# Performance work log

Hardware: AMD Instinct MI355X
Metric: run time of the kernel (lower is better)

Reference implementation:

```python
import jax, jax.numpy as jnp
import numpy as np

B, T, F, H, O = 256, 1024, 128, 512, 64
BN_EPS = 1e-5


def setup_inputs() -> dict:
    key = jax.random.key(0)
    ks = jax.random.split(key, 24)
    p = lambda k, shape: 0.02 * jax.random.normal(k, shape, dtype=jnp.float32)
    inp = {
        "x": jax.random.normal(ks[0], (B, T, F), dtype=jnp.float32),
        "delta": jax.random.uniform(ks[1], (B, T, F), dtype=jnp.float32),
        "m": (jax.random.uniform(ks[2], (B, T, F)) > 0.5).astype(jnp.float32),
        "x_forward": jax.random.normal(ks[3], (B, T, F), dtype=jnp.float32),
        # packed-sequence style: descending number of active rows per timestep
        "batch_sizes": jnp.sort(jax.random.randint(ks[4], (T,), 1, B + 1))[::-1].astype(jnp.int32),
        "W_r": p(ks[5], (F, H)), "U_r": p(ks[6], (H, H)), "V_r": p(ks[7], (F, H)), "b_r": jnp.zeros((H,), jnp.float32),
        "W_z": p(ks[8], (F, H)), "U_z": p(ks[9], (H, H)), "V_z": p(ks[10], (F, H)), "b_z": jnp.zeros((H,), jnp.float32),
        "W": p(ks[11], (F, H)), "U": p(ks[12], (H, H)), "V": p(ks[13], (F, H)), "b": jnp.zeros((H,), jnp.float32),
        "W_gamma_x": p(ks[14], (F,)), "b_gamma_x": jnp.zeros((F,), jnp.float32),
        "W_gamma_h": p(ks[15], (F, H)), "b_gamma_h": jnp.zeros((H,), jnp.float32),
        "dec_W": p(ks[16], (H, O)), "dec_b": jnp.zeros((O,), jnp.float32),
        "bn_w": jnp.ones((H,), jnp.float32), "bn_b": jnp.zeros((H,), jnp.float32),
    }
    return inp


def reference(x, delta, m, x_forward, batch_sizes,
              W_r, U_r, V_r, b_r, W_z, U_z, V_z, b_z, W, U, V, b,
              W_gamma_x, b_gamma_x, W_gamma_h, b_gamma_h,
              dec_W, dec_b, bn_w, bn_b):
    # input decay gamma_x: [B,T,F]; hidden decay gamma_h: [B,T,H]
    gamma_x = jnp.exp(-jax.nn.relu(delta * W_gamma_x + b_gamma_x))
    gamma_h = jnp.exp(-jax.nn.relu(jnp.einsum("btf,fh->bth", m, W_gamma_h) + b_gamma_h))
    # impute observed (m==1) positions with decayed forward-fill (matches x[m.byte()] = x_replace[m.byte()])
    x_rep = gamma_x * x_forward + (1.0 - gamma_x) * 0.001
    x = jnp.where(m > 0.5, x_rep, x)

    # time-major for scan
    xT = jnp.transpose(x, (1, 0, 2))        # [T,B,F]
    mT = jnp.transpose(m, (1, 0, 2))        # [T,B,F]
    gT = jnp.transpose(gamma_h, (1, 0, 2))  # [T,B,H]
    row = jnp.arange(B)

    def step(h, inp):
        x_t, m_t, g_t, bs = inp
        mask = (row < bs)[:, None]          # active rows this step
        h_d = jnp.where(mask, g_t * h, h)   # decayed hidden (index_copy_ on [:bs])
        one_m = 1.0 - m_t
        z = jax.nn.sigmoid(x_t @ W_z + h_d @ U_z + one_m @ V_z + b_z)
        r = jax.nn.sigmoid(x_t @ W_r + h_d @ U_r + one_m @ V_r + b_r)
        h_tilde = jnp.tanh(x_t @ W + (h_d * r) @ U + one_m @ V + b)
        h_new = jnp.where(mask, (1.0 - z) * h_d + z * h_tilde, h_d)
        return h_new, None

    h0 = jnp.zeros((B, H), jnp.float32)
    h_t, _ = jax.lax.scan(step, h0, (xT, mT, gT, batch_sizes))

    # eval-mode BatchNorm1d (running_mean=0, running_var=1); batch_size>1 so BN applies
    h_bn = h_t * (bn_w / jnp.sqrt(1.0 + BN_EPS)) + bn_b
    output = jax.nn.log_softmax(h_bn @ dec_W + dec_b, axis=-1)
    return output, h_bn
```

## Files before the change

### kernel.cpp

```cpp
#include <hip/hip_runtime.h>
#include <hip/hip_bf16.h>

typedef __attribute__((ext_vector_type(8))) short bf16x8;
typedef __attribute__((ext_vector_type(4))) float f32x4;
typedef __attribute__((ext_vector_type(4))) float fvec4;
typedef __attribute__((ext_vector_type(4))) unsigned short u16x4;
typedef __attribute__((ext_vector_type(4))) int i32x4;
typedef __attribute__((ext_vector_type(2))) unsigned int u32x2;

#define DEVI __device__ __forceinline__

constexpr int BB = 256, TT = 1024, FF = 128, HH = 512, OO = 64;
constexpr int KK = 256;
constexpr int NN = 2048;

DEVI unsigned short f2bf(float x) {
  unsigned int u = __float_as_uint(x);
  u += 0x7FFFu + ((u >> 16) & 1u);
  return (unsigned short)(u >> 16);
}
DEVI float bf2f(unsigned short s) {
  return __uint_as_float(((unsigned int)s) << 16);
}

DEVI void gload16(const void* g, void* lds) {
  __builtin_amdgcn_global_load_lds(
      (const __attribute__((address_space(1))) void*)g,
      (__attribute__((address_space(3))) void*)lds, 16, 0, 0);
}

DEVI void barrier_lds() {
  asm volatile("s_waitcnt lgkmcnt(0)" ::: "memory");
  __builtin_amdgcn_s_barrier();
  __builtin_amdgcn_sched_barrier(0);
}

DEVI int hgIdx(int row, int c) { return row*1024 + (c ^ ((row & 7) << 3)); }

__global__ __launch_bounds__(256) void prep_scales_kernel(
    const float* __restrict__ U_z, const float* __restrict__ U_r,
    const float* __restrict__ Uh, float* __restrict__ uscale)
{
  int n = blockIdx.x * 256 + threadIdx.x;
  if (n >= 1536) return;
  const float* src = (n < 512) ? U_z : (n < 1024) ? U_r : Uh;
  int col = n & 511;
  float s = 0.f;
  for (int k = 0; k < HH; ++k) s = fmaxf(s, fabsf(src[k*HH + col]));
  uscale[n] = fmaxf(s, 1e-30f);
}

__global__ __launch_bounds__(256) void prep_kernel(
    const float* __restrict__ W_z, const float* __restrict__ V_z, const float* __restrict__ b_z,
    const float* __restrict__ W_r, const float* __restrict__ V_r, const float* __restrict__ b_r,
    const float* __restrict__ Wh,  const float* __restrict__ Vh,  const float* __restrict__ bh,
    const float* __restrict__ Wgh, const float* __restrict__ bgh,
    const float* __restrict__ U_z, const float* __restrict__ U_r, const float* __restrict__ Uh,
    const float* __restrict__ uscale,
    unsigned short* __restrict__ BwT, float* __restrict__ bias,
    unsigned int* __restrict__ UzrN, unsigned int* __restrict__ UhN)
{
  int idx = blockIdx.x * 256 + threadIdx.x;
  if (idx < 524288) {
    int n = idx >> 8, k = idx & 255;
    float v;
    if (n < 512)       { int h = n;        v = (k < 128) ? W_z[k*HH + h] : -V_z[(k-128)*HH + h]; }
    else if (n < 1024) { int h = n - 512;  v = (k < 128) ? W_r[k*HH + h] : -V_r[(k-128)*HH + h]; }
    else if (n < 1536) { int h = n - 1024; v = (k < 128) ? Wh [k*HH + h] : -Vh [(k-128)*HH + h]; }
    else               { int h = n - 1536; v = (k < 128) ? 0.f : Wgh[(k-128)*HH + h]; }
    BwT[n*256 + k] = f2bf(v);
    return;
  }
  idx -= 524288;
  if (idx < 2048) {
    int n = idx; float v;
    if (n < 512)       { float s = b_z[n];      for (int f = 0; f < FF; ++f) s += V_z[f*HH + n];        v = s; }
    else if (n < 1024) { int h = n-512;  float s = b_r[h]; for (int f = 0; f < FF; ++f) s += V_r[f*HH + h]; v = s; }
    else if (n < 1536) { int h = n-1024; float s = bh[h];  for (int f = 0; f < FF; ++f) s += Vh[f*HH + h];  v = s; }
    else               { v = bgh[n-1536]; }
    bias[n] = v;
    return;
  }
  idx -= 2048;
  if (idx < 65536) {
    int c  = idx & 1;
    int l  = (idx >> 1) & 63;
    int i  = (idx >> 7) & 3;
    int wv = (idx >> 9) & 7;
    int u  = idx >> 12;
    int kt = u >> 1, half = u & 1;
    int col = (wv*4 + i)*16 + (l & 15);
    const float* src = half ? U_r : U_z;
    float sc = 7.f / uscale[half*512 + col];
    unsigned int word = 0;
#pragma unroll
    for (int p = 0; p < 8; ++p) {
      int j = c*8 + (p & 1)*4 + (p >> 1);
      int k = kt*64 + (l >> 4)*16 + j;
      float q = fminf(fmaxf(rintf(src[k*HH + col] * sc), -7.f), 7.f);
      unsigned int uq = (unsigned int)((int)q + 8);
      word |= (uq & 0xF) << (4*p);
    }
    UzrN[idx] = word;
    return;
  }
  idx -= 65536;
  if (idx < 32768) {
    int c  = idx & 1;
    int l  = (idx >> 1) & 63;
    int i  = (idx >> 7) & 3;
    int wv = (idx >> 9) & 7;
    int u  = idx >> 12;
    int col = (wv*4 + i)*16 + (l & 15);
    float sc = 7.f / uscale[1024 + col];
    unsigned int word = 0;
#pragma unroll
    for (int p = 0; p < 8; ++p) {
      int j = c*8 + (p & 1)*4 + (p >> 1);
      int k = u*64 + (l >> 4)*16 + j;
      float q = fminf(fmaxf(rintf(Uh[k*HH + col] * sc), -7.f), 7.f);
      unsigned int uq = (unsigned int)((int)q + 8);
      word |= (uq & 0xF) << (4*p);
    }
    UhN[idx] = word;
  }
}

__global__ __launch_bounds__(256) void build_A_kernel(
    const float* __restrict__ x, const float* __restrict__ delta,
    const float* __restrict__ mm, const float* __restrict__ xf,
    const float* __restrict__ Wgx, const float* __restrict__ bgx,
    const int* __restrict__ bs, unsigned short* __restrict__ A,
    int t0, int TC)
{
  int blk = blockIdx.x;
  int row8 = blk * 8;
  int b0  = row8 / TC;
  int tl0 = row8 % TC;
  if (b0 >= bs[t0 + tl0]) return;
  int tid = threadIdx.x;
  int rl = row8 + (tid >> 5);
  int tc = tl0 + (tid >> 5);
  long gi = ((long)b0*TT + t0 + tc) * 32 + (tid & 31);
  int f0 = (tid & 31) * 4;
  fvec4 xv = ((const fvec4*)x)[gi];
  fvec4 dv = ((const fvec4*)delta)[gi];
  fvec4 mv = ((const fvec4*)mm)[gi];
  fvec4 fv = ((const fvec4*)xf)[gi];
  unsigned short ox[4], om[4];
#pragma unroll
  for (int j = 0; j < 4; ++j) {
    float g  = __expf(-fmaxf(dv[j]*Wgx[f0+j] + bgx[f0+j], 0.f));
    float xr = g*fv[j] + (1.f - g)*0.001f;
    float xi = (mv[j] > 0.5f) ? xr : xv[j];
    ox[j] = f2bf(xi); om[j] = f2bf(mv[j]);
  }
  *(u16x4*)(A + (long)rl*KK + f0)       = (u16x4){ox[0], ox[1], ox[2], ox[3]};
  *(u16x4*)(A + (long)rl*KK + 128 + f0) = (u16x4){om[0], om[1], om[2], om[3]};
}

__global__ __launch_bounds__(256) void gemm1_kernel(
    const unsigned short* __restrict__ A, const unsigned short* __restrict__ BwT,
    const float* __restrict__ bias, const int* __restrict__ bs,
    unsigned short* __restrict__ PRE, int t0, int TC)
{
  int blk = blockIdx.x;
  int nt = blk & 15;
  int mt = blk >> 4;
  {
    int m0 = mt * 128;
    int b_ = m0 / TC;
    int bcheck = (TC >= 128) ? bs[t0 + (m0 % TC)] : bs[t0];
    if (b_ >= bcheck) return;
  }
  int tid = threadIdx.x;
  int w = tid >> 6, l = tid & 63;
  int wm = w >> 1, wn = w & 1;
  int lr = l & 15, lg = l >> 4;
  int m_base = mt*128 + wm*64;
  int n_base = nt*128 + wn*64;
  const unsigned short* Aptr = A   + (long)(m_base + lr)*KK + lg*8;
  const unsigned short* Bptr = BwT + (long)(n_base + lr)*KK + lg*8;
  f32x4 acc[4][4];
#pragma unroll
  for (int i = 0; i < 4; ++i)
#pragma unroll
    for (int j = 0; j < 4; ++j) acc[i][j] = (f32x4){0.f, 0.f, 0.f, 0.f};

#pragma unroll
  for (int kt = 0; kt < 8; ++kt) {
    bf16x8 af[4], bfr[4];
#pragma unroll
    for (int i = 0; i < 4; ++i) af[i]  = *(const bf16x8*)(Aptr + (long)i*16*KK + kt*32);
#pragma unroll
    for (int i = 0; i < 4; ++i) bfr[i] = *(const bf16x8*)(Bptr + (long)i*16*KK + kt*32);
#pragma unroll
    for (int ms = 0; ms < 4; ++ms)
#pragma unroll
      for (int ns = 0; ns < 4; ++ns)
        acc[ms][ns] = __builtin_amdgcn_mfma_f32_16x16x32_bf16(af[ms], bfr[ns], acc[ms][ns], 0, 0, 0);
  }
#pragma unroll
  for (int ms = 0; ms < 4; ++ms) {
    int gm0 = m_base + ms*16 + lg*4;
#pragma unroll
    for (int ns = 0; ns < 4; ++ns) {
      int gn = n_base + ns*16 + lr;
      float bv = bias[gn];
      bool is_gamma = (gn >= 1536);
#pragma unroll
      for (int q = 0; q < 4; ++q) {
        float v = acc[ms][ns][q] + bv;
        if (is_gamma) v = __expf(-fmaxf(v, 0.f));
        PRE[(long)(gm0 + q)*NN + gn] = f2bf(v);
      }
    }
  }
}

__global__ __launch_bounds__(512, 2) void scan_kernel(
    const unsigned short* __restrict__ PRE,
    const unsigned int* __restrict__ UzrN,
    const unsigned int* __restrict__ UhN,
    const float* __restrict__ uscale,
    const int* __restrict__ bs,
    float* __restrict__ h_st,
    float* __restrict__ sbuf,
    int t0, int TC)
{
  __shared__ __align__(16) char Ubuf[8][4][2048];
  __shared__ __align__(16) i32x4 hd_l[8*64];
  __shared__ __align__(16) unsigned short slabHG[16*1024];
  __shared__ float hm[16][524];
  __shared__ int hsumW[8][16];
  __shared__ int hsumW2[8][16];
  __shared__ float wmax[8];

  const int tid = threadIdx.x;
  const int r0 = blockIdx.x * 16;
  if (t0 > 0 && bs[t0] <= r0) return;

  const int w = tid >> 6, l = tid & 63, lr = l & 15, lg = l >> 4;
  const size_t rowStr = (size_t)TC * NN;

  auto STAGEB = [&](int u) {
    const char* src = (const char*)UhN + ((size_t)(u*8 + w))*2048 + (size_t)l*16;
    char* dst = &Ubuf[w][u & 3][0];
    gload16(src, dst);
    gload16(src + 1024, dst + 1024);
  };
  auto STAGEHG = [&](const unsigned short* PREn) {
#pragma unroll
    for (int j = 0; j < 4; ++j) {
      int idx = w*4 + j;
      int row = idx >> 1;
      int phys = (idx & 1)*512 + l*8;
      int logi = phys ^ ((row & 7) << 3);
      const unsigned short* src = PREn + (size_t)row*rowStr + 1024 + logi;
      gload16(src, &slabHG[idx*512]);
    }
  };
  auto LOADZR = [&](int u, u32x2* d) {
#pragma unroll
    for (int i = 0; i < 4; ++i)
      d[i] = ((const u32x2*)UzrN)[((u*8 + w)*4 + i)*64 + l];
  };

  float zdq[4], rdq[4], hdq[4];
#pragma unroll
  for (int i = 0; i < 4; ++i) {
    int c = (w*4 + i)*16 + lr;
    zdq[i] = uscale[c]        * (1.f/889.f);
    rdq[i] = uscale[512 + c]  * (1.f/889.f);
    hdq[i] = uscale[1024 + c] * (1.f/889.f);
  }
  if (tid < 8) wmax[tid] = (t0 == 0) ? 1e-20f : sbuf[blockIdx.x];

  if (t0 == 0) {
    for (int i = tid; i < 16*512; i += 512) hm[i>>9][i&511] = 0.f;
  } else {
    for (int i = tid; i < 16*512; i += 512)
      hm[i>>9][i&511] = h_st[(size_t)(r0 + (i>>9))*HH + (i&511)];
  }
  asm volatile("s_waitcnt vmcnt(0)" ::: "memory");
  __builtin_amdgcn_sched_barrier(0);

  STAGEHG(PRE + (size_t)r0*TC*NN);
  STAGEB(0); STAGEB(1);

  for (int tc = 0; tc < TC; ++tc) {
    const int bsv = bs[t0 + tc];
    if (bsv <= r0) break;
    const int na = min(16, bsv - r0);
    const unsigned short* PREstep = PRE + ((size_t)r0*TC + tc)*NN;
    const unsigned short* PREnext = PREstep + NN;

    barrier_lds();
    asm volatile("s_waitcnt vmcnt(4)" ::: "memory");
    __builtin_amdgcn_sched_barrier(0);

    float s = wmax[0];
#pragma unroll
    for (int i = 1; i < 8; ++i) s = fmaxf(s, wmax[i]);
    const float qs = 127.f / s;

    unsigned short pzr[2][4][4];
#pragma unroll
    for (int i = 0; i < 4; ++i)
#pragma unroll
      for (int q = 0; q < 4; ++q) {
        int row = lg*4 + q, col = (w*4 + i)*16 + lr;
        const unsigned short* pb = PREstep + (size_t)row*rowStr + col;
        pzr[0][i][q] = pb[0];
        pzr[1][i][q] = pb[512];
      }

    u32x2 inW[4][4];
    LOADZR(0, inW[0]); LOADZR(1, inW[1]);
    LOADZR(2, inW[2]); LOADZR(3, inW[3]);

    i32x4 qwReg;
    {
      const int k0 = w*64 + lg*16;
      const bool act = lr < na;
      bf16x8 g0 = *(const bf16x8*)&slabHG[hgIdx(lr, 512 + k0)];
      bf16x8 g1 = *(const bf16x8*)&slabHG[hgIdx(lr, 512 + k0 + 8)];
      int psum = 0;
#pragma unroll
      for (int d = 0; d < 4; ++d) {
        int word = 0;
#pragma unroll
        for (int b = 0; b < 4; ++b) {
          int j = d*4 + b;
          float h  = hm[lr][k0 + j];
          float gv = bf2f((unsigned short)(j < 8 ? g0[j] : g1[j-8]));
          float hd = act ? gv*h : h;
          float q  = fminf(fmaxf(rintf(hd*qs), -127.f), 127.f);
          int qi = (int)q;
          psum += qi;
          word |= (qi & 0xFF) << (8*b);
        }
        qwReg[d] = word;
      }
      hd_l[w*64 + l] = qwReg;
      psum += __shfl_xor(psum, 16);
      psum += __shfl_xor(psum, 32);
      if (lg == 0) hsumW[w][lr] = psum;
    }

    float phv[4][4], ggv[4][4];
#pragma unroll
    for (int i = 0; i < 4; ++i)
#pragma unroll
      for (int q = 0; q < 4; ++q) {
        int row = lg*4 + q, col = (w*4 + i)*16 + lr;
        phv[i][q] = bf2f(slabHG[hgIdx(row, col)]);
        ggv[i][q] = bf2f(slabHG[hgIdx(row, 512 + col)]);
      }
    barrier_lds();

    i32x4 acc[8];
#pragma unroll
    for (int i = 0; i < 8; ++i) acc[i] = (i32x4){0, 0, 0, 0};
    i32x4 af;
#pragma unroll
    for (int u = 0; u < 16; ++u) {
      if (!(u & 1)) af = hd_l[(u>>1)*64 + l];
      u32x2* inw = inW[u & 3];
      __builtin_amdgcn_s_setprio(1);
#pragma unroll
      for (int i = 0; i < 4; ++i) {
        unsigned int W0 = inw[i][0], W1 = inw[i][1];
        i32x4 bfr;
        bfr[0] = (int)(W0 & 0x0F0F0F0Fu);
        bfr[1] = (int)((W0 >> 4) & 0x0F0F0F0Fu);
        bfr[2] = (int)(W1 & 0x0F0F0F0Fu);
        bfr[3] = (int)((W1 >> 4) & 0x0F0F0F0Fu);
        acc[(u&1)*4 + i] = __builtin_amdgcn_mfma_i32_16x16x64_i8(af, bfr, acc[(u&1)*4 + i], 0, 0, 0);
      }
      __builtin_amdgcn_s_setprio(0);
      if (u < 12) LOADZR(u + 4, inW[u & 3]);
    }
    STAGEB(2); STAGEB(3);

    int rsum[4];
#pragma unroll
    for (int q = 0; q < 4; ++q) {
      int row = lg*4 + q, t = 0;
#pragma unroll
      for (int w2 = 0; w2 < 8; ++w2) t += hsumW[w2][row];
      rsum[q] = t * 8;
    }
    float zreg[4][4];
#pragma unroll
    for (int i = 0; i < 4; ++i)
#pragma unroll
      for (int q = 0; q < 4; ++q) {
        int row = lg*4 + q, col = (w*4 + i)*16 + lr;
        float az = bf2f(pzr[0][i][q]) + (float)(acc[i][q]   - rsum[q]) * zdq[i] * s;
        float ar = bf2f(pzr[1][i][q]) + (float)(acc[4+i][q] - rsum[q]) * rdq[i] * s;
        zreg[i][q] = 1.f/(1.f + __expf(-az));
        slabHG[hgIdx(row, col)] = f2bf(1.f/(1.f + __expf(-ar)));
      }
    barrier_lds();

    {
      const int k0 = w*64 + lg*16;
      bf16x8 r0v = *(const bf16x8*)&slabHG[hgIdx(lr, k0)];
      bf16x8 r1v = *(const bf16x8*)&slabHG[hgIdx(lr, k0 + 8)];
      i32x4 nw;
      int psum2 = 0;
#pragma unroll
      for (int d = 0; d < 4; ++d) {
        int word = qwReg[d], out = 0;
#pragma unroll
        for (int b = 0; b < 4; ++b) {
          int j = d*4 + b;
          int hq = (int)(signed char)((word >> (8*b)) & 0xFF);
          float rv = bf2f((unsigned short)(j < 8 ? r0v[j] : r1v[j-8]));
          float q = fminf(fmaxf(rintf((float)hq * rv), -127.f), 127.f);
          int qi = (int)q;
          psum2 += qi;
          out |= (qi & 0xFF) << (8*b);
        }
        nw[d] = out;
      }
      hd_l[w*64 + l] = nw;
      psum2 += __shfl_xor(psum2, 16);
      psum2 += __shfl_xor(psum2, 32);
      if (lg == 0) hsumW2[w][lr] = psum2;
    }
    barrier_lds();

    i32x4 accB[4];
#pragma unroll
    for (int i = 0; i < 4; ++i) accB[i] = (i32x4){0, 0, 0, 0};
#pragma unroll
    for (int u = 0; u < 8; ++u) {
      if (u < 5) { asm volatile("s_waitcnt vmcnt(6)" ::: "memory"); }
      else       { asm volatile("s_waitcnt vmcnt(8)" ::: "memory"); }
      __builtin_amdgcn_sched_barrier(0);
      const char* buf = &Ubuf[w][u & 3][0];
      i32x4 af2 = hd_l[u*64 + l];
      __builtin_amdgcn_s_setprio(1);
#pragma unroll
      for (int i = 0; i < 4; ++i) {
        u32x2 Wv = *(const u32x2*)&buf[(i*64 + l)*8];
        unsigned int W0 = Wv[0], W1 = Wv[1];
        i32x4 bfr;
        bfr[0] = (int)(W0 & 0x0F0F0F0Fu);
        bfr[1] = (int)((W0 >> 4) & 0x0F0F0F0Fu);
        bfr[2] = (int)(W1 & 0x0F0F0F0Fu);
        bfr[3] = (int)((W1 >> 4) & 0x0F0F0F0Fu);
        accB[i] = __builtin_amdgcn_mfma_i32_16x16x64_i8(af2, bfr, accB[i], 0, 0, 0);
      }
      __builtin_amdgcn_s_setprio(0);
      __builtin_amdgcn_sched_barrier(0);
      if (u < 4)       STAGEB(u + 4);
      else if (u == 4) STAGEHG(PREnext);
      else if (u == 5) STAGEB(0);
      else if (u == 6) STAGEB(1);
    }

    int rsum2[4];
#pragma unroll
    for (int q = 0; q < 4; ++q) {
      int row = lg*4 + q, t = 0;
#pragma unroll
      for (int w2 = 0; w2 < 8; ++w2) t += hsumW2[w2][row];
      rsum2[q] = t * 8;
    }
    float mloc = 0.f;
#pragma unroll
    for (int i = 0; i < 4; ++i)
#pragma unroll
      for (int q = 0; q < 4; ++q) {
        int row = lg*4 + q, col = (w*4 + i)*16 + lr;
        float hval;
        if (row < na) {
          float ah = phv[i][q] + (float)(accB[i][q] - rsum2[q]) * hdq[i] * s;
          float e  = __expf(2.f*ah);
          float th = 1.f - 2.f/(e + 1.f);
          float hd = ggv[i][q] * hm[row][col];
          hval = hd + zreg[i][q]*(th - hd);
          hm[row][col] = hval;
        } else {
          hval = hm[row][col];
        }
        mloc = fmaxf(mloc, fabsf(hval));
      }
#pragma unroll
    for (int off = 32; off > 0; off >>= 1) mloc = fmaxf(mloc, __shfl_xor(mloc, off));
    if (l == 0) wmax[w] = fmaxf(mloc, 1e-20f);
  }

  asm volatile("s_waitcnt vmcnt(0)" ::: "memory");
  barrier_lds();
  for (int i = tid; i < 16*512; i += 512)
    h_st[(size_t)(r0 + (i>>9))*HH + (i&511)] = hm[i>>9][i&511];
  if (tid == 0) {
    float s = wmax[0];
#pragma unroll
    for (int i = 1; i < 8; ++i) s = fmaxf(s, wmax[i]);
    sbuf[blockIdx.x] = s;
  }
}

__global__ __launch_bounds__(64) void head_kernel(
    const float* __restrict__ h_state, const float* __restrict__ decW,
    const float* __restrict__ decb, const float* __restrict__ bnw,
    const float* __restrict__ bnb, float* __restrict__ out)
{
  int b = blockIdx.x, o = threadIdx.x;
  __shared__ float hbn[HH];
  const float s = rsqrtf(1.f + 1e-5f);
  for (int j = o; j < HH; j += 64)
    hbn[j] = h_state[(long)b*HH + j] * (bnw[j] * s) + bnb[j];
  __syncthreads();
  float acc = decb[o];
  for (int j = 0; j < HH; ++j) acc += hbn[j] * decW[j*OO + o];
  float mx = acc;
#pragma unroll
  for (int off = 32; off > 0; off >>= 1) mx = fmaxf(mx, __shfl_xor(mx, off));
  float ex = __expf(acc - mx);
  float sum = ex;
#pragma unroll
  for (int off = 32; off > 0; off >>= 1) sum += __shfl_xor(sum, off);
  out[(long)b*OO + o] = acc - mx - __logf(sum);
  for (int j = o; j < HH; j += 64)
    out[(long)BB*OO + (long)b*HH + j] = hbn[j];
}

extern "C" void kernel_launch(void* const* d_in, const int* in_sizes, int n_in,
                              void* d_out, int out_size, void* d_ws, size_t ws_size,
                              hipStream_t stream) {
  const float* x     = (const float*)d_in[0];
  const float* delta = (const float*)d_in[1];
  const float* mm    = (const float*)d_in[2];
  const float* xf    = (const float*)d_in[3];
  const int*   bs    = (const int*)  d_in[4];
  const float* W_r   = (const float*)d_in[5];
  const float* U_r   = (const float*)d_in[6];
  const float* V_r   = (const float*)d_in[7];
  const float* b_r   = (const float*)d_in[8];
  const float* W_z   = (const float*)d_in[9];
  const float* U_z   = (const float*)d_in[10];
  const float* V_z   = (const float*)d_in[11];
  const float* b_z   = (const float*)d_in[12];
  const float* W     = (const float*)d_in[13];
  const float* U     = (const float*)d_in[14];
  const float* V     = (const float*)d_in[15];
  const float* b     = (const float*)d_in[16];
  const float* Wgx   = (const float*)d_in[17];
  const float* bgx   = (const float*)d_in[18];
  const float* Wgh   = (const float*)d_in[19];
  const float* bgh   = (const float*)d_in[20];
  const float* decW  = (const float*)d_in[21];
  const float* decb  = (const float*)d_in[22];
  const float* bnw   = (const float*)d_in[23];
  const float* bnb   = (const float*)d_in[24];

  auto rnd = [](size_t v) { return (v + 255) & ~(size_t)255; };
  const size_t fixed_bytes = rnd((size_t)2048*256*2) + rnd(2048*4)
                           + rnd((size_t)256*1024) + rnd((size_t)128*1024)
                           + rnd(1536*4) + rnd(64)
                           + rnd((size_t)BB*HH*4);
  int TC = 0;
  const int cands[5] = {128, 64, 32, 16, 8};
  for (int i = 0; i < 5; ++i) {
    size_t need = fixed_bytes + rnd((size_t)BB*cands[i]*KK*2) + rnd((size_t)BB*cands[i]*NN*2);
    if (need <= ws_size) { TC = cands[i]; break; }
  }
  if (TC == 0) return;

  char* p = (char*)d_ws;
  auto alloc = [&](size_t bytes) { char* r = p; p += (bytes + 255) & ~(size_t)255; return r; };
  unsigned short* A_chunk = (unsigned short*)alloc((size_t)BB * TC * KK * 2);
  unsigned short* PREc    = (unsigned short*)alloc((size_t)BB * TC * NN * 2);
  unsigned short* BwT     = (unsigned short*)alloc((size_t)2048 * 256 * 2);
  float*          bias    = (float*)alloc(2048 * 4);
  unsigned int*   UzrN    = (unsigned int*)alloc((size_t)256 * 1024);
  unsigned int*   UhN     = (unsigned int*)alloc((size_t)128 * 1024);
  float*          uscale  = (float*)alloc(1536 * 4);
  float*          sbuf    = (float*)alloc(64);
  float*          h_st    = (float*)alloc((size_t)BB * HH * 4);

  prep_scales_kernel<<<6, 256, 0, stream>>>(U_z, U_r, U, uscale);
  prep_kernel<<<2440, 256, 0, stream>>>(W_z, V_z, b_z, W_r, V_r, b_r, W, V, b,
                                        Wgh, bgh, U_z, U_r, U, uscale,
                                        BwT, bias, UzrN, UhN);
  const int nch = TT / TC;
  for (int c = 0; c < nch; ++c) {
    int t0 = c * TC;
    build_A_kernel<<<BB*TC/8, 256, 0, stream>>>(x, delta, mm, xf, Wgx, bgx, bs,
                                                A_chunk, t0, TC);
    gemm1_kernel<<<(BB*TC/128)*16, 256, 0, stream>>>(A_chunk, BwT, bias, bs,
                                                     PREc, t0, TC);
    scan_kernel<<<16, 512, 0, stream>>>(PREc, UzrN, UhN, uscale, bs,
                                        h_st, sbuf, t0, TC);
  }
  head_kernel<<<256, 64, 0, stream>>>(h_st, decW, decb, bnw, bnb, (float*)d_out);
}
```

Measured before the change: 19.58 ms.

## Stream U_h weights directly into registers instead of LDS staging buffers

Removes the per-wave LDS staging buffer for the U_h int4 weights and instead loads them straight from global memory into registers, prefetching two steps ahead and interleaved with the z/r MFMA loop. The z/r weight prefetch is restructured into a copy-then-reload register rotation. The top-of-step wait now drains all memory counters before the barrier, and the clamp to ±127 in requantization is dropped. This cuts LDS footprint and LDS traffic and may raise occupancy, at the cost of more VGPRs and a full vmcnt(0) stall each step. Removing the clamp risks int8 wraparound if values exceed the range.

```diff
diff --git a/kernel.cpp b/kernel.cpp
--- a/kernel.cpp
+++ b/kernel.cpp
@@ -228,7 +228,6 @@
     float* __restrict__ sbuf,
     int t0, int TC)
 {
-  __shared__ __align__(16) char Ubuf[8][4][2048];
   __shared__ __align__(16) i32x4 hd_l[8*64];
   __shared__ __align__(16) unsigned short slabHG[16*1024];
   __shared__ float hm[16][524];
@@ -243,12 +242,6 @@
   const int w = tid >> 6, l = tid & 63, lr = l & 15, lg = l >> 4;
   const size_t rowStr = (size_t)TC * NN;
 
-  auto STAGEB = [&](int u) {
-    const char* src = (const char*)UhN + ((size_t)(u*8 + w))*2048 + (size_t)l*16;
-    char* dst = &Ubuf[w][u & 3][0];
-    gload16(src, dst);
-    gload16(src + 1024, dst + 1024);
-  };
   auto STAGEHG = [&](const unsigned short* PREn) {
 #pragma unroll
     for (int j = 0; j < 4; ++j) {
@@ -263,7 +256,12 @@
   auto LOADZR = [&](int u, u32x2* d) {
 #pragma unroll
     for (int i = 0; i < 4; ++i)
-      d[i] = ((const u32x2*)UzrN)[((u*8 + w)*4 + i)*64 + l];
+      d[i] = ((const u32x2*)UzrN)[(u*8 + w)*256 + i*64 + l];
+  };
+  auto LOADB = [&](int u, u32x2* d) {
+#pragma unroll
+    for (int i = 0; i < 4; ++i)
+      d[i] = ((const u32x2*)UhN)[(u*8 + w)*256 + i*64 + l];
   };
 
   float zdq[4], rdq[4], hdq[4];
@@ -286,7 +284,9 @@
   __builtin_amdgcn_sched_barrier(0);
 
   STAGEHG(PRE + (size_t)r0*TC*NN);
-  STAGEB(0); STAGEB(1);
+
+  u32x2 inZ[4][4];
+  u32x2 inB[2][4];
 
   for (int tc = 0; tc < TC; ++tc) {
     const int bsv = bs[t0 + tc];
@@ -295,8 +295,9 @@
     const unsigned short* PREstep = PRE + ((size_t)r0*TC + tc)*NN;
     const unsigned short* PREnext = PREstep + NN;
 
-    barrier_lds();
-    asm volatile("s_waitcnt vmcnt(4)" ::: "memory");
+    asm volatile("s_waitcnt lgkmcnt(0)" ::: "memory");
+    asm volatile("s_waitcnt vmcnt(0)" ::: "memory");
+    __builtin_amdgcn_s_barrier();
     __builtin_amdgcn_sched_barrier(0);
 
     float s = wmax[0];
@@ -315,9 +316,8 @@
         pzr[1][i][q] = pb[512];
       }
 
-    u32x2 inW[4][4];
-    LOADZR(0, inW[0]); LOADZR(1, inW[1]);
-    LOADZR(2, inW[2]); LOADZR(3, inW[3]);
+    LOADZR(0, inZ[0]); LOADZR(1, inZ[1]);
+    LOADZR(2, inZ[2]); LOADZR(3, inZ[3]);
 
     i32x4 qwReg;
     {
@@ -335,8 +335,7 @@
           float h  = hm[lr][k0 + j];
           float gv = bf2f((unsigned short)(j < 8 ? g0[j] : g1[j-8]));
           float hd = act ? gv*h : h;
-          float q  = fminf(fmaxf(rintf(hd*qs), -127.f), 127.f);
-          int qi = (int)q;
+          int qi = (int)rintf(hd*qs);
           psum += qi;
           word |= (qi & 0xFF) << (8*b);
         }
@@ -366,11 +365,16 @@
 #pragma unroll
     for (int u = 0; u < 16; ++u) {
       if (!(u & 1)) af = hd_l[(u>>1)*64 + l];
-      u32x2* inw = inW[u & 3];
+      u32x2 cur[4];
+#pragma unroll
+      for (int i = 0; i < 4; ++i) cur[i] = inZ[u & 3][i];
+      if (u < 12)       LOADZR(u + 4, inZ[u & 3]);
+      else if (u == 14) LOADB(0, inB[0]);
+      else if (u == 15) LOADB(1, inB[1]);
       __builtin_amdgcn_s_setprio(1);
 #pragma unroll
       for (int i = 0; i < 4; ++i) {
-        unsigned int W0 = inw[i][0], W1 = inw[i][1];
+        unsigned int W0 = cur[i][0], W1 = cur[i][1];
         i32x4 bfr;
         bfr[0] = (int)(W0 & 0x0F0F0F0Fu);
         bfr[1] = (int)((W0 >> 4) & 0x0F0F0F0Fu);
@@ -379,9 +383,7 @@
         acc[(u&1)*4 + i] = __builtin_amdgcn_mfma_i32_16x16x64_i8(af, bfr, acc[(u&1)*4 + i], 0, 0, 0);
       }
       __builtin_amdgcn_s_setprio(0);
-      if (u < 12) LOADZR(u + 4, inW[u & 3]);
-    }
-    STAGEB(2); STAGEB(3);
+    }
 
     int rsum[4];
 #pragma unroll
@@ -418,8 +420,7 @@
           int j = d*4 + b;
           int hq = (int)(signed char)((word >> (8*b)) & 0xFF);
           float rv = bf2f((unsigned short)(j < 8 ? r0v[j] : r1v[j-8]));
-          float q = fminf(fmaxf(rintf((float)hq * rv), -127.f), 127.f);
-          int qi = (int)q;
+          int qi = (int)rintf((float)hq * rv);
           psum2 += qi;
           out |= (qi & 0xFF) << (8*b);
         }
@@ -437,16 +438,16 @@
     for (int i = 0; i < 4; ++i) accB[i] = (i32x4){0, 0, 0, 0};
 #pragma unroll
     for (int u = 0; u < 8; ++u) {
-      if (u < 5) { asm volatile("s_waitcnt vmcnt(6)" ::: "memory"); }
-      else       { asm volatile("s_waitcnt vmcnt(8)" ::: "memory"); }
-      __builtin_amdgcn_sched_barrier(0);
-      const char* buf = &Ubuf[w][u & 3][0];
+      u32x2 cur[4];
+#pragma unroll
+      for (int i = 0; i < 4; ++i) cur[i] = inB[u & 1][i];
+      if (u < 6)       LOADB(u + 2, inB[u & 1]);
+      if (u == 4)      STAGEHG(PREnext);
       i32x4 af2 = hd_l[u*64 + l];
       __builtin_amdgcn_s_setprio(1);
 #pragma unroll
       for (int i = 0; i < 4; ++i) {
-        u32x2 Wv = *(const u32x2*)&buf[(i*64 + l)*8];
-        unsigned int W0 = Wv[0], W1 = Wv[1];
+        unsigned int W0 = cur[i][0], W1 = cur[i][1];
         i32x4 bfr;
         bfr[0] = (int)(W0 & 0x0F0F0F0Fu);
         bfr[1] = (int)((W0 >> 4) & 0x0F0F0F0Fu);
@@ -455,11 +456,6 @@
         accB[i] = __builtin_amdgcn_mfma_i32_16x16x64_i8(af2, bfr, accB[i], 0, 0, 0);
       }
       __builtin_amdgcn_s_setprio(0);
-      __builtin_amdgcn_sched_barrier(0);
-      if (u < 4)       STAGEB(u + 4);
-      else if (u == 4) STAGEHG(PREnext);
-      else if (u == 5) STAGEB(0);
-      else if (u == 6) STAGEB(1);
     }
 
     int rsum2[4];
```

After: 25.10 ms. +28.2%, slower.

## Double scan kernel block to 1024 threads, halving per-wave column tiles

Applied to the files above, without the earlier changes.

The recurrent scan kernel now runs 16 waves per block instead of 8. Each wave owns two 16-column tiles instead of four, and the weight packing layout is reindexed to match. The aim is to cut the serial per-timestep latency by spreading the int8/int4 MFMA work and gate math over more waves. In exchange, the quantisation and h_d packing stages run on only half the waves, barriers span more waves, and the int8 clamp was dropped, which risks overflow if a value rounds past 127.

```diff
diff --git a/kernel.cpp b/kernel.cpp
--- a/kernel.cpp
+++ b/kernel.cpp
@@ -85,11 +85,10 @@
   if (idx < 65536) {
     int c  = idx & 1;
     int l  = (idx >> 1) & 63;
-    int i  = (idx >> 7) & 3;
-    int wv = (idx >> 9) & 7;
+    int t  = (idx >> 7) & 31;
     int u  = idx >> 12;
     int kt = u >> 1, half = u & 1;
-    int col = (wv*4 + i)*16 + (l & 15);
+    int col = t*16 + (l & 15);
     const float* src = half ? U_r : U_z;
     float sc = 7.f / uscale[half*512 + col];
     unsigned int word = 0;
@@ -108,10 +107,9 @@
   if (idx < 32768) {
     int c  = idx & 1;
     int l  = (idx >> 1) & 63;
-    int i  = (idx >> 7) & 3;
-    int wv = (idx >> 9) & 7;
+    int t  = (idx >> 7) & 31;
     int u  = idx >> 12;
-    int col = (wv*4 + i)*16 + (l & 15);
+    int col = t*16 + (l & 15);
     float sc = 7.f / uscale[1024 + col];
     unsigned int word = 0;
 #pragma unroll
@@ -218,7 +216,7 @@
   }
 }
 
-__global__ __launch_bounds__(512, 2) void scan_kernel(
+__global__ __launch_bounds__(1024) void scan_kernel(
     const unsigned short* __restrict__ PRE,
     const unsigned int* __restrict__ UzrN,
     const unsigned int* __restrict__ UhN,
@@ -228,13 +226,13 @@
     float* __restrict__ sbuf,
     int t0, int TC)
 {
-  __shared__ __align__(16) char Ubuf[8][4][2048];
+  __shared__ __align__(16) char Ubuf[16][4][1024];
   __shared__ __align__(16) i32x4 hd_l[8*64];
   __shared__ __align__(16) unsigned short slabHG[16*1024];
   __shared__ float hm[16][524];
   __shared__ int hsumW[8][16];
   __shared__ int hsumW2[8][16];
-  __shared__ float wmax[8];
+  __shared__ float wmax[16];
 
   const int tid = threadIdx.x;
   const int r0 = blockIdx.x * 16;
@@ -244,42 +242,38 @@
   const size_t rowStr = (size_t)TC * NN;
 
   auto STAGEB = [&](int u) {
-    const char* src = (const char*)UhN + ((size_t)(u*8 + w))*2048 + (size_t)l*16;
-    char* dst = &Ubuf[w][u & 3][0];
-    gload16(src, dst);
-    gload16(src + 1024, dst + 1024);
+    const char* src = (const char*)UhN + ((size_t)(u*32 + w*2))*512 + (size_t)l*16;
+    gload16(src, &Ubuf[w][u & 3][0]);
   };
   auto STAGEHG = [&](const unsigned short* PREn) {
 #pragma unroll
-    for (int j = 0; j < 4; ++j) {
-      int idx = w*4 + j;
-      int row = idx >> 1;
-      int phys = (idx & 1)*512 + l*8;
-      int logi = phys ^ ((row & 7) << 3);
-      const unsigned short* src = PREn + (size_t)row*rowStr + 1024 + logi;
-      gload16(src, &slabHG[idx*512]);
+    for (int j = 0; j < 2; ++j) {
+      int phys = j*512 + l*8;
+      int logi = phys ^ ((w & 7) << 3);
+      const unsigned short* src = PREn + (size_t)w*rowStr + 1024 + logi;
+      gload16(src, &slabHG[(w*2 + j)*512]);
     }
   };
   auto LOADZR = [&](int u, u32x2* d) {
 #pragma unroll
-    for (int i = 0; i < 4; ++i)
-      d[i] = ((const u32x2*)UzrN)[((u*8 + w)*4 + i)*64 + l];
+    for (int i = 0; i < 2; ++i)
+      d[i] = ((const u32x2*)UzrN)[(u*32 + w*2 + i)*64 + l];
   };
 
-  float zdq[4], rdq[4], hdq[4];
-#pragma unroll
-  for (int i = 0; i < 4; ++i) {
-    int c = (w*4 + i)*16 + lr;
+  float zdq[2], rdq[2], hdq[2];
+#pragma unroll
+  for (int i = 0; i < 2; ++i) {
+    int c = (w*2 + i)*16 + lr;
     zdq[i] = uscale[c]        * (1.f/889.f);
     rdq[i] = uscale[512 + c]  * (1.f/889.f);
     hdq[i] = uscale[1024 + c] * (1.f/889.f);
   }
-  if (tid < 8) wmax[tid] = (t0 == 0) ? 1e-20f : sbuf[blockIdx.x];
+  if (tid < 16) wmax[tid] = (t0 == 0) ? 1e-20f : sbuf[blockIdx.x];
 
   if (t0 == 0) {
-    for (int i = tid; i < 16*512; i += 512) hm[i>>9][i&511] = 0.f;
+    for (int i = tid; i < 16*512; i += 1024) hm[i>>9][i&511] = 0.f;
   } else {
-    for (int i = tid; i < 16*512; i += 512)
+    for (int i = tid; i < 16*512; i += 1024)
       hm[i>>9][i&511] = h_st[(size_t)(r0 + (i>>9))*HH + (i&511)];
   }
   asm volatile("s_waitcnt vmcnt(0)" ::: "memory");
@@ -287,6 +281,8 @@
 
   STAGEHG(PRE + (size_t)r0*TC*NN);
   STAGEB(0); STAGEB(1);
+
+  u32x2 inZ[4][2];
 
   for (int tc = 0; tc < TC; ++tc) {
     const int bsv = bs[t0 + tc];
@@ -296,31 +292,30 @@
     const unsigned short* PREnext = PREstep + NN;
 
     barrier_lds();
-    asm volatile("s_waitcnt vmcnt(4)" ::: "memory");
+    asm volatile("s_waitcnt vmcnt(2)" ::: "memory");
     __builtin_amdgcn_sched_barrier(0);
 
     float s = wmax[0];
 #pragma unroll
-    for (int i = 1; i < 8; ++i) s = fmaxf(s, wmax[i]);
+    for (int i = 1; i < 16; ++i) s = fmaxf(s, wmax[i]);
     const float qs = 127.f / s;
 
-    unsigned short pzr[2][4][4];
-#pragma unroll
-    for (int i = 0; i < 4; ++i)
+    unsigned short pzr[2][2][4];
+#pragma unroll
+    for (int i = 0; i < 2; ++i)
 #pragma unroll
       for (int q = 0; q < 4; ++q) {
-        int row = lg*4 + q, col = (w*4 + i)*16 + lr;
+        int row = lg*4 + q, col = (w*2 + i)*16 + lr;
         const unsigned short* pb = PREstep + (size_t)row*rowStr + col;
         pzr[0][i][q] = pb[0];
         pzr[1][i][q] = pb[512];
       }
 
-    u32x2 inW[4][4];
-    LOADZR(0, inW[0]); LOADZR(1, inW[1]);
-    LOADZR(2, inW[2]); LOADZR(3, inW[3]);
+    LOADZR(0, inZ[0]); LOADZR(1, inZ[1]);
+    LOADZR(2, inZ[2]); LOADZR(3, inZ[3]);
 
     i32x4 qwReg;
-    {
+    if (w < 8) {
       const int k0 = w*64 + lg*16;
       const bool act = lr < na;
       bf16x8 g0 = *(const bf16x8*)&slabHG[hgIdx(lr, 512 + k0)];
@@ -335,8 +330,7 @@
           float h  = hm[lr][k0 + j];
           float gv = bf2f((unsigned short)(j < 8 ? g0[j] : g1[j-8]));
           float hd = act ? gv*h : h;
-          float q  = fminf(fmaxf(rintf(hd*qs), -127.f), 127.f);
-          int qi = (int)q;
+          int qi = (int)rintf(hd*qs);
           psum += qi;
           word |= (qi & 0xFF) << (8*b);
         }
@@ -348,38 +342,37 @@
       if (lg == 0) hsumW[w][lr] = psum;
     }
 
-    float phv[4][4], ggv[4][4];
-#pragma unroll
-    for (int i = 0; i < 4; ++i)
+    float phv[2][4], ggv[2][4];
+#pragma unroll
+    for (int i = 0; i < 2; ++i)
 #pragma unroll
       for (int q = 0; q < 4; ++q) {
-        int row = lg*4 + q, col = (w*4 + i)*16 + lr;
+        int row = lg*4 + q, col = (w*2 + i)*16 + lr;
         phv[i][q] = bf2f(slabHG[hgIdx(row, col)]);
         ggv[i][q] = bf2f(slabHG[hgIdx(row, 512 + col)]);
       }
     barrier_lds();
 
-    i32x4 acc[8];
-#pragma unroll
-    for (int i = 0; i < 8; ++i) acc[i] = (i32x4){0, 0, 0, 0};
+    i32x4 acc[4];
+#pragma unroll
+    for (int i = 0; i < 4; ++i) acc[i] = (i32x4){0, 0, 0, 0};
     i32x4 af;
 #pragma unroll
     for (int u = 0; u < 16; ++u) {
       if (!(u & 1)) af = hd_l[(u>>1)*64 + l];
-      u32x2* inw = inW[u & 3];
       __builtin_amdgcn_s_setprio(1);
 #pragma unroll
-      for (int i = 0; i < 4; ++i) {
-        unsigned int W0 = inw[i][0], W1 = inw[i][1];
+      for (int i = 0; i < 2; ++i) {
+        unsigned int W0 = inZ[u & 3][i][0], W1 = inZ[u & 3][i][1];
         i32x4 bfr;
         bfr[0] = (int)(W0 & 0x0F0F0F0Fu);
         bfr[1] = (int)((W0 >> 4) & 0x0F0F0F0Fu);
         bfr[2] = (int)(W1 & 0x0F0F0F0Fu);
         bfr[3] = (int)((W1 >> 4) & 0x0F0F0F0Fu);
-        acc[(u&1)*4 + i] = __builtin_amdgcn_mfma_i32_16x16x64_i8(af, bfr, acc[(u&1)*4 + i], 0, 0, 0);
+        acc[(u&1)*2 + i] = __builtin_amdgcn_mfma_i32_16x16x64_i8(af, bfr, acc[(u&1)*2 + i], 0, 0, 0);
       }
       __builtin_amdgcn_s_setprio(0);
-      if (u < 12) LOADZR(u + 4, inW[u & 3]);
+      if (u < 12) LOADZR(u + 4, inZ[u & 3]);
     }
     STAGEB(2); STAGEB(3);
 
@@ -391,20 +384,20 @@
       for (int w2 = 0; w2 < 8; ++w2) t += hsumW[w2][row];
       rsum[q] = t * 8;
     }
-    float zreg[4][4];
-#pragma unroll
-    for (int i = 0; i < 4; ++i)
+    float zreg[2][4];
+#pragma unroll
+    for (int i = 0; i < 2; ++i)
 #pragma unroll
       for (int q = 0; q < 4; ++q) {
-        int row = lg*4 + q, col = (w*4 + i)*16 + lr;
+        int row = lg*4 + q, col = (w*2 + i)*16 + lr;
         float az = bf2f(pzr[0][i][q]) + (float)(acc[i][q]   - rsum[q]) * zdq[i] * s;
-        float ar = bf2f(pzr[1][i][q]) + (float)(acc[4+i][q] - rsum[q]) * rdq[i] * s;
+        float ar = bf2f(pzr[1][i][q]) + (float)(acc[2+i][q] - rsum[q]) * rdq[i] * s;
         zreg[i][q] = 1.f/(1.f + __expf(-az));
         slabHG[hgIdx(row, col)] = f2bf(1.f/(1.f + __expf(-ar)));
       }
     barrier_lds();
 
-    {
+    if (w < 8) {
       const int k0 = w*64 + lg*16;
       bf16x8 r0v = *(const bf16x8*)&slabHG[hgIdx(lr, k0)];
       bf16x8 r1v = *(const bf16x8*)&slabHG[hgIdx(lr, k0 + 8)];
@@ -418,8 +411,7 @@
           int j = d*4 + b;
           int hq = (int)(signed char)((word >> (8*b)) & 0xFF);
           float rv = bf2f((unsigned short)(j < 8 ? r0v[j] : r1v[j-8]));
-          float q = fminf(fmaxf(rintf((float)hq * rv), -127.f), 127.f);
-          int qi = (int)q;
+          int qi = (int)rintf((float)hq * rv);
           psum2 += qi;
           out |= (qi & 0xFF) << (8*b);
         }
@@ -432,20 +424,20 @@
     }
     barrier_lds();
 
-    i32x4 accB[4];
-#pragma unroll
-    for (int i = 0; i < 4; ++i) accB[i] = (i32x4){0, 0, 0, 0};
+    i32x4 accB[2];
+#pragma unroll
+    for (int i = 0; i < 2; ++i) accB[i] = (i32x4){0, 0, 0, 0};
 #pragma unroll
     for (int u = 0; u < 8; ++u) {
-      if (u < 5) { asm volatile("s_waitcnt vmcnt(6)" ::: "memory"); }
-      else       { asm volatile("s_waitcnt vmcnt(8)" ::: "memory"); }
+      if (u < 5) { asm volatile("s_waitcnt vmcnt(3)" ::: "memory"); }
+      else       { asm volatile("s_waitcnt vmcnt(4)" ::: "memory"); }
       __builtin_amdgcn_sched_barrier(0);
       const char* buf = &Ubuf[w][u & 3][0];
       i32x4 af2 = hd_l[u*64 + l];
       __builtin_amdgcn_s_setprio(1);
 #pragma unroll
-      for (int i = 0; i < 4; ++i) {
-        u32x2 Wv = *(const u32x2*)&buf[(i*64 + l)*8];
+      for (int i = 0; i < 2; ++i) {
+        u32x2 Wv = *(const u32x2*)&buf[i*512 + l*8];
         unsigned int W0 = Wv[0], W1 = Wv[1];
         i32x4 bfr;
         bfr[0] = (int)(W0 & 0x0F0F0F0Fu);
@@ -472,10 +464,10 @@
     }
     float mloc = 0.f;
 #pragma unroll
-    for (int i = 0; i < 4; ++i)
+    for (int i = 0; i < 2; ++i)
 #pragma unroll
       for (int q = 0; q < 4; ++q) {
-        int row = lg*4 + q, col = (w*4 + i)*16 + lr;
+        int row = lg*4 + q, col = (w*2 + i)*16 + lr;
         float hval;
         if (row < na) {
           float ah = phv[i][q] + (float)(accB[i][q] - rsum2[q]) * hdq[i] * s;
@@ -496,12 +488,12 @@
 
   asm volatile("s_waitcnt vmcnt(0)" ::: "memory");
   barrier_lds();
-  for (int i = tid; i < 16*512; i += 512)
+  for (int i = tid; i < 16*512; i += 1024)
     h_st[(size_t)(r0 + (i>>9))*HH + (i&511)] = hm[i>>9][i&511];
   if (tid == 0) {
     float s = wmax[0];
 #pragma unroll
-    for (int i = 1; i < 8; ++i) s = fmaxf(s, wmax[i]);
+    for (int i = 1; i < 16; ++i) s = fmaxf(s, wmax[i]);
     sbuf[blockIdx.x] = s;
   }
 }
@@ -596,8 +588,8 @@
                                                 A_chunk, t0, TC);
     gemm1_kernel<<<(BB*TC/128)*16, 256, 0, stream>>>(A_chunk, BwT, bias, bs,
                                                      PREc, t0, TC);
-    scan_kernel<<<16, 512, 0, stream>>>(PREc, UzrN, UhN, uscale, bs,
-                                        h_st, sbuf, t0, TC);
+    scan_kernel<<<16, 1024, 0, stream>>>(PREc, UzrN, UhN, uscale, bs,
+                                         h_st, sbuf, t0, TC);
   }
   head_kernel<<<256, 64, 0, stream>>>(h_st, decW, decb, bnw, bnb, (float*)d_out);
 }
```

Result: slower. 23.18 ms (+18.4%).

## Prefetch next step's Uzr weights across timesteps and trim scan barriers

Applied to the files above, without the earlier changes.

Moves the first four Uzr weight-chunk register loads from the start of each timestep to the end of the previous one, so their global latency overlaps the tail of the step. A separate LDS buffer for the r-scaled activations replaces the workgroup barrier after the r-gate writes with a local lgkmcnt wait, and the top-of-loop wait is rewritten to match the extra outstanding loads. The clamp to ±127 during quantisation is dropped, which relies on the scale keeping values in range. Risks include higher register pressure, a missed LDS hazard where slabHG is written by other waves and then read across waves without a barrier, and vmcnt counts that may no longer match the loads in flight.

```diff
diff --git a/kernel.cpp b/kernel.cpp
--- a/kernel.cpp
+++ b/kernel.cpp
@@ -230,6 +230,7 @@
 {
   __shared__ __align__(16) char Ubuf[8][4][2048];
   __shared__ __align__(16) i32x4 hd_l[8*64];
+  __shared__ __align__(16) i32x4 a2_l[8*64];
   __shared__ __align__(16) unsigned short slabHG[16*1024];
   __shared__ float hm[16][524];
   __shared__ int hsumW[8][16];
@@ -263,7 +264,7 @@
   auto LOADZR = [&](int u, u32x2* d) {
 #pragma unroll
     for (int i = 0; i < 4; ++i)
-      d[i] = ((const u32x2*)UzrN)[((u*8 + w)*4 + i)*64 + l];
+      d[i] = ((const u32x2*)UzrN)[(u*8 + w)*256 + i*64 + l];
   };
 
   float zdq[4], rdq[4], hdq[4];
@@ -285,8 +286,12 @@
   asm volatile("s_waitcnt vmcnt(0)" ::: "memory");
   __builtin_amdgcn_sched_barrier(0);
 
+  u32x2 inZ[4][4];
   STAGEHG(PRE + (size_t)r0*TC*NN);
   STAGEB(0); STAGEB(1);
+  __builtin_amdgcn_sched_barrier(0);
+  LOADZR(0, inZ[0]); LOADZR(1, inZ[1]);
+  LOADZR(2, inZ[2]); LOADZR(3, inZ[3]);
 
   for (int tc = 0; tc < TC; ++tc) {
     const int bsv = bs[t0 + tc];
@@ -295,8 +300,9 @@
     const unsigned short* PREstep = PRE + ((size_t)r0*TC + tc)*NN;
     const unsigned short* PREnext = PREstep + NN;
 
-    barrier_lds();
-    asm volatile("s_waitcnt vmcnt(4)" ::: "memory");
+    asm volatile("s_waitcnt lgkmcnt(0)" ::: "memory");
+    asm volatile("s_waitcnt vmcnt(20)" ::: "memory");
+    __builtin_amdgcn_s_barrier();
     __builtin_amdgcn_sched_barrier(0);
 
     float s = wmax[0];
@@ -314,10 +320,6 @@
         pzr[0][i][q] = pb[0];
         pzr[1][i][q] = pb[512];
       }
-
-    u32x2 inW[4][4];
-    LOADZR(0, inW[0]); LOADZR(1, inW[1]);
-    LOADZR(2, inW[2]); LOADZR(3, inW[3]);
 
     i32x4 qwReg;
     {
@@ -335,8 +337,7 @@
           float h  = hm[lr][k0 + j];
           float gv = bf2f((unsigned short)(j < 8 ? g0[j] : g1[j-8]));
           float hd = act ? gv*h : h;
-          float q  = fminf(fmaxf(rintf(hd*qs), -127.f), 127.f);
-          int qi = (int)q;
+          int qi = (int)rintf(hd*qs);
           psum += qi;
           word |= (qi & 0xFF) << (8*b);
         }
@@ -366,11 +367,10 @@
 #pragma unroll
     for (int u = 0; u < 16; ++u) {
       if (!(u & 1)) af = hd_l[(u>>1)*64 + l];
-      u32x2* inw = inW[u & 3];
       __builtin_amdgcn_s_setprio(1);
 #pragma unroll
       for (int i = 0; i < 4; ++i) {
-        unsigned int W0 = inw[i][0], W1 = inw[i][1];
+        unsigned int W0 = inZ[u & 3][i][0], W1 = inZ[u & 3][i][1];
         i32x4 bfr;
         bfr[0] = (int)(W0 & 0x0F0F0F0Fu);
         bfr[1] = (int)((W0 >> 4) & 0x0F0F0F0Fu);
@@ -379,7 +379,7 @@
         acc[(u&1)*4 + i] = __builtin_amdgcn_mfma_i32_16x16x64_i8(af, bfr, acc[(u&1)*4 + i], 0, 0, 0);
       }
       __builtin_amdgcn_s_setprio(0);
-      if (u < 12) LOADZR(u + 4, inW[u & 3]);
+      if (u < 12) LOADZR(u + 4, inZ[u & 3]);
     }
     STAGEB(2); STAGEB(3);
 
@@ -402,7 +402,8 @@
         zreg[i][q] = 1.f/(1.f + __expf(-az));
         slabHG[hgIdx(row, col)] = f2bf(1.f/(1.f + __expf(-ar)));
       }
-    barrier_lds();
+    asm volatile("s_waitcnt lgkmcnt(0)" ::: "memory");
+    __builtin_amdgcn_sched_barrier(0);
 
     {
       const int k0 = w*64 + lg*16;
@@ -418,14 +419,13 @@
           int j = d*4 + b;
           int hq = (int)(signed char)((word >> (8*b)) & 0xFF);
           float rv = bf2f((unsigned short)(j < 8 ? r0v[j] : r1v[j-8]));
-          float q = fminf(fmaxf(rintf((float)hq * rv), -127.f), 127.f);
-          int qi = (int)q;
+          int qi = (int)rintf((float)hq * rv);
           psum2 += qi;
           out |= (qi & 0xFF) << (8*b);
         }
         nw[d] = out;
       }
-      hd_l[w*64 + l] = nw;
+      a2_l[w*64 + l] = nw;
       psum2 += __shfl_xor(psum2, 16);
       psum2 += __shfl_xor(psum2, 32);
       if (lg == 0) hsumW2[w][lr] = psum2;
@@ -441,7 +441,7 @@
       else       { asm volatile("s_waitcnt vmcnt(8)" ::: "memory"); }
       __builtin_amdgcn_sched_barrier(0);
       const char* buf = &Ubuf[w][u & 3][0];
-      i32x4 af2 = hd_l[u*64 + l];
+      i32x4 af2 = a2_l[u*64 + l];
       __builtin_amdgcn_s_setprio(1);
 #pragma unroll
       for (int i = 0; i < 4; ++i) {
@@ -461,6 +461,10 @@
       else if (u == 5) STAGEB(0);
       else if (u == 6) STAGEB(1);
     }
+    __builtin_amdgcn_sched_barrier(0);
+    LOADZR(0, inZ[0]); LOADZR(1, inZ[1]);
+    LOADZR(2, inZ[2]); LOADZR(3, inZ[3]);
+    __builtin_amdgcn_sched_barrier(0);
 
     int rsum2[4];
 #pragma unroll
```

Result: slower. 22.81 ms (+16.5%).
